# Performance work log

Hardware: AMD Instinct MI355X
Metric: run time of the kernel (lower is better)

The kernel has to match this reference:

```python
import jax, jax.numpy as jnp
import numpy as np

N, E = 20000, 320000          # nodes, edges
R, B = 9, 9                   # num_relations, num_bases
IN, HID, OUT = 128, 256, 64   # feature dims
EPS = 1e-5                    # LayerNorm eps


def layer_norm(h, gamma, beta):
    mu = jnp.mean(h, axis=-1, keepdims=True)
    var = jnp.var(h, axis=-1, keepdims=True)
    return (h - mu) * jax.lax.rsqrt(var + EPS) * gamma + beta


def rgcn_conv(x, src, dst, etype, bases, comp, root, bias, aggr):
    # basis decomposition: W_r = sum_b comp[r,b] * bases[b]
    W = jnp.einsum('rb,bio->rio', comp, bases)          # [R, in, out]
    xW = jnp.einsum('ni,rio->rno', x, W)                # [R, N, out]
    msg = xW[etype, src]                                # [E, out] gather per edge
    if aggr == 'max':
        agg = jax.ops.segment_max(msg, dst, num_segments=N)
        agg = jnp.where(jnp.isfinite(agg), agg, 0.0)    # empty segments -> 0
    else:
        agg = jax.ops.segment_sum(msg, dst, num_segments=N)
    return agg + x @ root + bias


def setup_inputs() -> dict:
    key = jax.random.key(0)
    ks = jax.random.split(key, 12)
    rn = lambda k, s, sc=0.05: jax.random.normal(k, s, jnp.float32) * sc
    return {
        'x': jax.random.normal(ks[0], (N, IN), jnp.float32),
        'edge_index': jax.random.randint(ks[1], (2, E), 0, N),
        'edge_type': jax.random.randint(ks[2], (E,), 0, R),
        # conv1 params
        'bases1': rn(ks[3], (B, IN, HID)),
        'comp1': rn(ks[4], (R, B), 0.3),
        'root1': rn(ks[5], (IN, HID)),
        'bias1': jnp.zeros((HID,), jnp.float32),
        'g1': jnp.ones((HID,), jnp.float32),
        'b1': jnp.zeros((HID,), jnp.float32),
        # conv2 params
        'bases2': rn(ks[6], (B, HID, OUT)),
        'comp2': rn(ks[7], (R, B), 0.3),
        'root2': rn(ks[8], (HID, OUT)),
        'bias2': jnp.zeros((OUT,), jnp.float32),
        'g2': jnp.ones((OUT,), jnp.float32),
        'b2': jnp.zeros((OUT,), jnp.float32),
    }


def reference(x, edge_index, edge_type, bases1, comp1, root1, bias1, g1, b1,
              bases2, comp2, root2, bias2, g2, b2):
    src, dst = edge_index[0], edge_index[1]
    h = rgcn_conv(x, src, dst, edge_type, bases1, comp1, root1, bias1, 'max')
    h = jax.nn.relu(layer_norm(h, g1, b1))
    # eval mode: edge dropout and feature dropout are identity
    h = rgcn_conv(h, src, dst, edge_type, bases2, comp2, root2, bias2, 'add')
    h = layer_norm(h, g2, b2)
    return jax.nn.log_softmax(h, axis=1)
```

## Files before the change

### kernel.cpp

```cpp
#include <hip/hip_runtime.h>
#include <math.h>

#define NN 20000
#define NE 320000
#define NREL 9
#define NBASES 9
#define D_IN 128
#define D_HID 256
#define D_OUT 64
#define LN_EPS 1e-5f

#define N1 (NREL * D_HID + D_HID)
#define N2 (NREL * D_OUT + D_OUT)
#define NBLK ((NN + 255) / 256)

typedef __attribute__((ext_vector_type(8))) short bf16x8;
typedef __attribute__((ext_vector_type(4))) float f32x4;

__device__ inline ushort f2b(float f) {
    unsigned u = __float_as_uint(f);
    return (ushort)((u + 0x7FFFu + ((u >> 16) & 1u)) >> 16);
}
__device__ inline float b2f(ushort h) { return __uint_as_float(((unsigned)h) << 16); }

__global__ __launch_bounds__(256) void prep_all(
    const float* __restrict__ bases1, const float* __restrict__ comp1, const float* __restrict__ root1,
    const float* __restrict__ bases2, const float* __restrict__ comp2, const float* __restrict__ root2,
    const float* __restrict__ x,
    ushort* __restrict__ w1t, ushort* __restrict__ w2t, ushort* __restrict__ xbf)
{
    const int SZ1 = N1 * D_IN;
    const int SZ2 = N2 * D_HID;
    const int SZX = NN * D_IN;
    int tid = blockIdx.x * 256 + threadIdx.x;
    if (tid < SZ1) {
        int n = tid >> 7, k = tid & 127;
        float s;
        if (n < NREL * D_HID) {
            int r = n >> 8, o = n & 255;
            s = 0.f;
            #pragma unroll
            for (int b = 0; b < NBASES; b++)
                s += comp1[r * NBASES + b] * bases1[(b * D_IN + k) * D_HID + o];
        } else {
            s = root1[k * D_HID + (n - NREL * D_HID)];
        }
        w1t[tid] = f2b(s);
    } else if (tid < SZ1 + SZ2) {
        int j = tid - SZ1;
        int n = j >> 8, k = j & 255;
        float s;
        if (n < NREL * D_OUT) {
            int r = n >> 6, o = n & 63;
            s = 0.f;
            #pragma unroll
            for (int b = 0; b < NBASES; b++)
                s += comp2[r * NBASES + b] * bases2[(b * D_HID + k) * D_OUT + o];
        } else {
            s = root2[k * D_OUT + (n - NREL * D_OUT)];
        }
        w2t[j] = f2b(s);
    } else if (tid < SZ1 + SZ2 + SZX) {
        int j = tid - SZ1 - SZ2;
        xbf[j] = f2b(x[j]);
    }
}

__global__ __launch_bounds__(256) void hist_dst(const int* __restrict__ dst, int* __restrict__ deg)
{
    int e = blockIdx.x * 256 + threadIdx.x;
    if (e < NE) atomicAdd(&deg[dst[e]], 1);
}

__global__ __launch_bounds__(256) void scan_blk(
    const int* __restrict__ deg, int* __restrict__ local, int* __restrict__ bsum)
{
    __shared__ int wsum[4];
    int tid = threadIdx.x, lane = tid & 63, w = tid >> 6;
    int i = blockIdx.x * 256 + tid;
    int v = (i < NN) ? deg[i] : 0;
    int x = v;
    #pragma unroll
    for (int d = 1; d < 64; d <<= 1) {
        int y = __shfl_up(x, d, 64);
        if (lane >= d) x += y;
    }
    if (lane == 63) wsum[w] = x;
    __syncthreads();
    int woff = 0;
    for (int j = 0; j < w; j++) woff += wsum[j];
    if (i < NN) local[i] = woff + x - v;
    if (tid == 255) bsum[blockIdx.x] = woff + x;
}

__global__ __launch_bounds__(64) void scan_top(const int* __restrict__ bsum, int* __restrict__ boff)
{
    int lane = threadIdx.x;
    int carry = 0;
    for (int base = 0; base < NBLK; base += 64) {
        int i = base + lane;
        int v = (i < NBLK) ? bsum[i] : 0;
        int x = v;
        #pragma unroll
        for (int d = 1; d < 64; d <<= 1) {
            int y = __shfl_up(x, d, 64);
            if (lane >= d) x += y;
        }
        if (i < NBLK) boff[i] = carry + x - v;
        carry += __shfl(x, 63, 64);
    }
}

__global__ __launch_bounds__(256) void scan_fin(
    const int* __restrict__ local, const int* __restrict__ boff,
    int* __restrict__ offs, int* __restrict__ cursor)
{
    int i = blockIdx.x * 256 + threadIdx.x;
    if (i < NN) {
        int o = local[i] + boff[i >> 8];
        offs[i] = o;
        cursor[i] = o;
    }
    if (i == NN) offs[NN] = NE;
}

__global__ __launch_bounds__(256) void scatter_ep(
    const int* __restrict__ src, const int* __restrict__ dst, const int* __restrict__ etype,
    int* __restrict__ cursor, int* __restrict__ ep1, int* __restrict__ ep2)
{
    int e = blockIdx.x * 256 + threadIdx.x;
    if (e >= NE) return;
    int d = dst[e];
    int s = src[e], r = etype[e];
    int pos = atomicAdd(&cursor[d], 1);
    ep1[pos] = s * N1 + r * D_HID;
    ep2[pos] = s * N2 + r * D_OUT;
}

__global__ __launch_bounds__(256) void gemm_bf16(
    const ushort* __restrict__ A, const ushort* __restrict__ Bt, ushort* __restrict__ C,
    int M, int N, int K)
{
    __shared__ ushort As[128 * 32];
    __shared__ ushort Bs[128 * 32];

    int tid = threadIdx.x;
    int lane = tid & 63, w = tid >> 6;
    int row0 = blockIdx.y * 128, col0 = blockIdx.x * 128;

    f32x4 acc[4][4];
    #pragma unroll
    for (int mt = 0; mt < 4; mt++)
        #pragma unroll
        for (int nt = 0; nt < 4; nt++)
            acc[mt][nt] = (f32x4){0.f, 0.f, 0.f, 0.f};

    for (int k0 = 0; k0 < K; k0 += 32) {
        #pragma unroll
        for (int cc = 0; cc < 2; cc++) {
            int c = tid + cc * 256;
            int m = c >> 2, kq = c & 3;
            int off = ((m >> 4) * 64 + (m & 15) + kq * 16) * 8;
            bf16x8 va = {0, 0, 0, 0, 0, 0, 0, 0};
            int gm = row0 + m;
            if (gm < M) va = *(const bf16x8*)&A[(size_t)gm * K + k0 + kq * 8];
            *(bf16x8*)&As[off] = va;
            bf16x8 vb = *(const bf16x8*)&Bt[(size_t)(col0 + m) * K + k0 + kq * 8];
            *(bf16x8*)&Bs[off] = vb;
        }
        __syncthreads();

        int tA = (w >> 1) * 4, tB = (w & 1) * 4;
        bf16x8 af[4], bfr[4];
        #pragma unroll
        for (int i = 0; i < 4; i++) af[i]  = *(const bf16x8*)&As[((tA + i) * 64 + lane) * 8];
        #pragma unroll
        for (int i = 0; i < 4; i++) bfr[i] = *(const bf16x8*)&Bs[((tB + i) * 64 + lane) * 8];

        #pragma unroll
        for (int mt = 0; mt < 4; mt++)
            #pragma unroll
            for (int nt = 0; nt < 4; nt++)
                acc[mt][nt] = __builtin_amdgcn_mfma_f32_16x16x32_bf16(af[mt], bfr[nt], acc[mt][nt], 0, 0, 0);
        __syncthreads();
    }

    int q = lane >> 4, cn = lane & 15;
    #pragma unroll
    for (int mt = 0; mt < 4; mt++) {
        #pragma unroll
        for (int i = 0; i < 4; i++) {
            int gr = row0 + (w >> 1) * 64 + mt * 16 + q * 4 + i;
            if (gr < M) {
                #pragma unroll
                for (int nt = 0; nt < 4; nt++) {
                    int gc = col0 + (w & 1) * 64 + nt * 16 + cn;
                    C[(size_t)gr * N + gc] = f2b(acc[mt][nt][i]);
                }
            }
        }
    }
}

__global__ __launch_bounds__(256) void gather1(
    const ushort* __restrict__ xw1, const int* __restrict__ offs, const int* __restrict__ ep1,
    const float* __restrict__ bias, const float* __restrict__ g, const float* __restrict__ b,
    ushort* __restrict__ h)
{
    int n = blockIdx.x * 4 + (threadIdx.x >> 6);
    if (n >= NN) return;
    int lane = threadIdx.x & 63;
    int lane4 = lane * 4;
    int e0 = __builtin_amdgcn_readfirstlane(offs[n]);
    int e1 = __builtin_amdgcn_readfirstlane(offs[n + 1]);

    float m0 = -INFINITY, m1 = -INFINITY, m2 = -INFINITY, m3 = -INFINITY;
    int e = e0;
    for (; e + 4 <= e1; e += 4) {
        int p0 = ep1[e + 0], p1 = ep1[e + 1], p2 = ep1[e + 2], p3 = ep1[e + 3];
        ushort4 v0 = *(const ushort4*)&xw1[(size_t)(p0 + lane4)];
        ushort4 v1 = *(const ushort4*)&xw1[(size_t)(p1 + lane4)];
        ushort4 v2 = *(const ushort4*)&xw1[(size_t)(p2 + lane4)];
        ushort4 v3 = *(const ushort4*)&xw1[(size_t)(p3 + lane4)];
        m0 = fmaxf(fmaxf(m0, fmaxf(b2f(v0.x), b2f(v1.x))), fmaxf(b2f(v2.x), b2f(v3.x)));
        m1 = fmaxf(fmaxf(m1, fmaxf(b2f(v0.y), b2f(v1.y))), fmaxf(b2f(v2.y), b2f(v3.y)));
        m2 = fmaxf(fmaxf(m2, fmaxf(b2f(v0.z), b2f(v1.z))), fmaxf(b2f(v2.z), b2f(v3.z)));
        m3 = fmaxf(fmaxf(m3, fmaxf(b2f(v0.w), b2f(v1.w))), fmaxf(b2f(v2.w), b2f(v3.w)));
    }
    for (; e < e1; e++) {
        int p = ep1[e];
        ushort4 v = *(const ushort4*)&xw1[(size_t)(p + lane4)];
        m0 = fmaxf(m0, b2f(v.x)); m1 = fmaxf(m1, b2f(v.y));
        m2 = fmaxf(m2, b2f(v.z)); m3 = fmaxf(m3, b2f(v.w));
    }
    if (e1 == e0) { m0 = m1 = m2 = m3 = 0.f; }

    ushort4 rt = *(const ushort4*)&xw1[(size_t)n * N1 + NREL * D_HID + lane4];
    int c = lane4;
    float t0 = m0 + b2f(rt.x) + bias[c + 0];
    float t1 = m1 + b2f(rt.y) + bias[c + 1];
    float t2 = m2 + b2f(rt.z) + bias[c + 2];
    float t3 = m3 + b2f(rt.w) + bias[c + 3];

    float s = t0 + t1 + t2 + t3;
    float s2 = t0 * t0 + t1 * t1 + t2 * t2 + t3 * t3;
    #pragma unroll
    for (int m = 32; m >= 1; m >>= 1) {
        s  += __shfl_xor(s,  m, 64);
        s2 += __shfl_xor(s2, m, 64);
    }
    float mu = s * (1.f / D_HID);
    float var = s2 * (1.f / D_HID) - mu * mu;
    float rs = rsqrtf(var + LN_EPS);

    ushort4 o;
    o.x = f2b(fmaxf((t0 - mu) * rs * g[c + 0] + b[c + 0], 0.f));
    o.y = f2b(fmaxf((t1 - mu) * rs * g[c + 1] + b[c + 1], 0.f));
    o.z = f2b(fmaxf((t2 - mu) * rs * g[c + 2] + b[c + 2], 0.f));
    o.w = f2b(fmaxf((t3 - mu) * rs * g[c + 3] + b[c + 3], 0.f));
    *(ushort4*)&h[(size_t)n * D_HID + c] = o;
}

__global__ __launch_bounds__(256) void gather2(
    const ushort* __restrict__ xw2, const int* __restrict__ offs, const int* __restrict__ ep2,
    const float* __restrict__ bias, const float* __restrict__ g, const float* __restrict__ b,
    float* __restrict__ out)
{
    int n = blockIdx.x * 4 + (threadIdx.x >> 6);
    if (n >= NN) return;
    int lane = threadIdx.x & 63;
    int e0 = __builtin_amdgcn_readfirstlane(offs[n]);
    int e1 = __builtin_amdgcn_readfirstlane(offs[n + 1]);

    float s = 0.f;
    int e = e0;
    for (; e + 4 <= e1; e += 4) {
        int p0 = ep2[e + 0], p1 = ep2[e + 1], p2 = ep2[e + 2], p3 = ep2[e + 3];
        float a0 = b2f(xw2[(size_t)(p0 + lane)]);
        float a1 = b2f(xw2[(size_t)(p1 + lane)]);
        float a2 = b2f(xw2[(size_t)(p2 + lane)]);
        float a3 = b2f(xw2[(size_t)(p3 + lane)]);
        s += (a0 + a1) + (a2 + a3);
    }
    for (; e < e1; e++) {
        s += b2f(xw2[(size_t)(ep2[e] + lane)]);
    }
    float v = s + b2f(xw2[(size_t)n * N2 + NREL * D_OUT + lane]) + bias[lane];

    float sm = v, s2 = v * v;
    #pragma unroll
    for (int m = 32; m >= 1; m >>= 1) {
        sm += __shfl_xor(sm, m, 64);
        s2 += __shfl_xor(s2, m, 64);
    }
    float mu = sm * (1.f / D_OUT);
    float var = s2 * (1.f / D_OUT) - mu * mu;
    float y = (v - mu) * rsqrtf(var + LN_EPS) * g[lane] + b[lane];

    float mx = y;
    #pragma unroll
    for (int m = 32; m >= 1; m >>= 1) mx = fmaxf(mx, __shfl_xor(mx, m, 64));
    float ex = __expf(y - mx);
    float se = ex;
    #pragma unroll
    for (int m = 32; m >= 1; m >>= 1) se += __shfl_xor(se, m, 64);
    out[(size_t)n * D_OUT + lane] = y - mx - logf(se);
}

extern "C" void kernel_launch(void* const* d_in, const int* in_sizes, int n_in,
                              void* d_out, int out_size, void* d_ws, size_t ws_size,
                              hipStream_t stream)
{
    const float* x      = (const float*)d_in[0];
    const int*   eidx   = (const int*)  d_in[1];
    const int*   etype  = (const int*)  d_in[2];
    const float* bases1 = (const float*)d_in[3];
    const float* comp1  = (const float*)d_in[4];
    const float* root1  = (const float*)d_in[5];
    const float* bias1  = (const float*)d_in[6];
    const float* g1     = (const float*)d_in[7];
    const float* b1     = (const float*)d_in[8];
    const float* bases2 = (const float*)d_in[9];
    const float* comp2  = (const float*)d_in[10];
    const float* root2  = (const float*)d_in[11];
    const float* bias2  = (const float*)d_in[12];
    const float* g2     = (const float*)d_in[13];
    const float* b2     = (const float*)d_in[14];

    const int* src = eidx;
    const int* dst = eidx + NE;

    char* p = (char*)d_ws;
    auto alloc = [&](size_t bytes) -> char* {
        char* r = p;
        p += (bytes + 255) & ~(size_t)255;
        return r;
    };
    ushort* xbf    = (ushort*)alloc((size_t)NN * D_IN * 2);
    ushort* w1t    = (ushort*)alloc((size_t)N1 * D_IN * 2);
    ushort* w2t    = (ushort*)alloc((size_t)N2 * D_HID * 2);
    ushort* xw1    = (ushort*)alloc((size_t)NN * N1 * 2);
    ushort* xw2    = (ushort*)alloc((size_t)NN * N2 * 2);
    ushort* h      = (ushort*)alloc((size_t)NN * D_HID * 2);
    int*    deg    = (int*)   alloc((size_t)NN * 4);
    int*    local  = (int*)   alloc((size_t)NN * 4);
    int*    bsum   = (int*)   alloc((size_t)NBLK * 4);
    int*    boff   = (int*)   alloc((size_t)NBLK * 4);
    int*    offs   = (int*)   alloc((size_t)(NN + 1) * 4);
    int*    cursor = (int*)   alloc((size_t)NN * 4);
    int*    ep1    = (int*)   alloc((size_t)NE * 4);
    int*    ep2    = (int*)   alloc((size_t)NE * 4);

    const int SZP = N1 * D_IN + N2 * D_HID + NN * D_IN;
    prep_all<<<(SZP + 255) / 256, 256, 0, stream>>>(
        bases1, comp1, root1, bases2, comp2, root2, x, w1t, w2t, xbf);

    hipMemsetAsync(deg, 0, (size_t)NN * 4, stream);
    hist_dst<<<(NE + 255) / 256, 256, 0, stream>>>(dst, deg);
    scan_blk<<<NBLK, 256, 0, stream>>>(deg, local, bsum);
    scan_top<<<1, 64, 0, stream>>>(bsum, boff);
    scan_fin<<<NBLK, 256, 0, stream>>>(local, boff, offs, cursor);
    scatter_ep<<<(NE + 255) / 256, 256, 0, stream>>>(src, dst, etype, cursor, ep1, ep2);

    gemm_bf16<<<dim3(N1 / 128, (NN + 127) / 128), 256, 0, stream>>>(xbf, w1t, xw1, NN, N1, D_IN);
    gather1<<<(NN + 3) / 4, 256, 0, stream>>>(xw1, offs, ep1, bias1, g1, b1, h);

    gemm_bf16<<<dim3(N2 / 128, (NN + 127) / 128), 256, 0, stream>>>(h, w2t, xw2, NN, N2, D_HID);
    gather2<<<(NN + 3) / 4, 256, 0, stream>>>(xw2, offs, ep2, bias2, g2, b2, (float*)d_out);
}
```

Before: 251.6 us.

## Use direct global-to-LDS loads, K=64 tiles and vectorized transposed GEMM epilogue

The bf16 GEMM now stages A and B tiles with global_load_lds (direct global-to-LDS DMA) instead of loading through registers, and doubles the K step per iteration to 64 so there are half as many barriers. The MFMA operands are swapped so each lane holds four consecutive output columns, which allows packed 8-byte stores in place of scalar 2-byte stores. Out-of-range rows are clamped to M-1 rather than zero-filled, which is safe because those rows are never stored. The LDS layout still has no swizzle, so bank conflicts on the fragment reads may remain.

```diff
diff --git a/kernel.cpp b/kernel.cpp
--- a/kernel.cpp
+++ b/kernel.cpp
@@ -22,6 +22,9 @@
     return (ushort)((u + 0x7FFFu + ((u >> 16) & 1u)) >> 16);
 }
 __device__ inline float b2f(ushort h) { return __uint_as_float(((unsigned)h) << 16); }
+__device__ inline unsigned pack2bf(float f0, float f1) {
+    return (unsigned)f2b(f0) | ((unsigned)f2b(f1) << 16);
+}
 
 __global__ __launch_bounds__(256) void prep_all(
     const float* __restrict__ bases1, const float* __restrict__ comp1, const float* __restrict__ root1,
@@ -141,11 +144,12 @@
     const ushort* __restrict__ A, const ushort* __restrict__ Bt, ushort* __restrict__ C,
     int M, int N, int K)
 {
-    __shared__ ushort As[128 * 32];
-    __shared__ ushort Bs[128 * 32];
+    __shared__ ushort As[1024 * 8];
+    __shared__ ushort Bs[1024 * 8];
 
     int tid = threadIdx.x;
     int lane = tid & 63, w = tid >> 6;
+    int wm = w >> 1, wn = w & 1;
     int row0 = blockIdx.y * 128, col0 = blockIdx.x * 128;
 
     f32x4 acc[4][4];
@@ -155,48 +159,68 @@
         for (int nt = 0; nt < 4; nt++)
             acc[mt][nt] = (f32x4){0.f, 0.f, 0.f, 0.f};
 
-    for (int k0 = 0; k0 < K; k0 += 32) {
-        #pragma unroll
-        for (int cc = 0; cc < 2; cc++) {
-            int c = tid + cc * 256;
-            int m = c >> 2, kq = c & 3;
-            int off = ((m >> 4) * 64 + (m & 15) + kq * 16) * 8;
-            bf16x8 va = {0, 0, 0, 0, 0, 0, 0, 0};
-            int gm = row0 + m;
-            if (gm < M) va = *(const bf16x8*)&A[(size_t)gm * K + k0 + kq * 8];
-            *(bf16x8*)&As[off] = va;
-            bf16x8 vb = *(const bf16x8*)&Bt[(size_t)(col0 + m) * K + k0 + kq * 8];
-            *(bf16x8*)&Bs[off] = vb;
+    for (int k0 = 0; k0 < K; k0 += 64) {
+        #pragma unroll
+        for (int it = 0; it < 4; it++) {
+            int sbase = (it * 4 + w) * 64;
+            int s = sbase + lane;
+            int g = s >> 7, rem = s & 127;
+            int kc = rem >> 4, mr = rem & 15;
+            int row = row0 + g * 16 + mr;
+            row = min(row, M - 1);
+            const ushort* ga = &A[(size_t)row * K + k0 + kc * 8];
+            __builtin_amdgcn_global_load_lds(
+                (const __attribute__((address_space(1))) unsigned int*)ga,
+                (__attribute__((address_space(3))) unsigned int*)&As[(size_t)sbase * 8],
+                16, 0, 0);
+        }
+        #pragma unroll
+        for (int it = 0; it < 4; it++) {
+            int sbase = (it * 4 + w) * 64;
+            int s = sbase + lane;
+            int g = s >> 7, rem = s & 127;
+            int kc = rem >> 4, mr = rem & 15;
+            int col = col0 + g * 16 + mr;
+            const ushort* gb = &Bt[(size_t)col * K + k0 + kc * 8];
+            __builtin_amdgcn_global_load_lds(
+                (const __attribute__((address_space(1))) unsigned int*)gb,
+                (__attribute__((address_space(3))) unsigned int*)&Bs[(size_t)sbase * 8],
+                16, 0, 0);
         }
         __syncthreads();
 
-        int tA = (w >> 1) * 4, tB = (w & 1) * 4;
-        bf16x8 af[4], bfr[4];
-        #pragma unroll
-        for (int i = 0; i < 4; i++) af[i]  = *(const bf16x8*)&As[((tA + i) * 64 + lane) * 8];
-        #pragma unroll
-        for (int i = 0; i < 4; i++) bfr[i] = *(const bf16x8*)&Bs[((tB + i) * 64 + lane) * 8];
-
-        #pragma unroll
-        for (int mt = 0; mt < 4; mt++)
+        #pragma unroll
+        for (int ks = 0; ks < 2; ks++) {
+            int fo = (ks * 4 + (lane >> 4)) * 16 + (lane & 15);
+            bf16x8 af[4], bfr[4];
+            #pragma unroll
+            for (int mt = 0; mt < 4; mt++)
+                af[mt] = *(const bf16x8*)&As[(size_t)(((wm * 4 + mt) * 128) + fo) * 8];
             #pragma unroll
             for (int nt = 0; nt < 4; nt++)
-                acc[mt][nt] = __builtin_amdgcn_mfma_f32_16x16x32_bf16(af[mt], bfr[nt], acc[mt][nt], 0, 0, 0);
+                bfr[nt] = *(const bf16x8*)&Bs[(size_t)(((wn * 4 + nt) * 128) + fo) * 8];
+            #pragma unroll
+            for (int mt = 0; mt < 4; mt++)
+                #pragma unroll
+                for (int nt = 0; nt < 4; nt++)
+                    acc[mt][nt] = __builtin_amdgcn_mfma_f32_16x16x32_bf16(
+                        bfr[nt], af[mt], acc[mt][nt], 0, 0, 0);
+        }
         __syncthreads();
     }
 
-    int q = lane >> 4, cn = lane & 15;
+    int q = lane >> 4, cm = lane & 15;
     #pragma unroll
     for (int mt = 0; mt < 4; mt++) {
-        #pragma unroll
-        for (int i = 0; i < 4; i++) {
-            int gr = row0 + (w >> 1) * 64 + mt * 16 + q * 4 + i;
-            if (gr < M) {
-                #pragma unroll
-                for (int nt = 0; nt < 4; nt++) {
-                    int gc = col0 + (w & 1) * 64 + nt * 16 + cn;
-                    C[(size_t)gr * N + gc] = f2b(acc[mt][nt][i]);
-                }
+        int gr = row0 + wm * 64 + mt * 16 + cm;
+        if (gr < M) {
+            #pragma unroll
+            for (int nt = 0; nt < 4; nt++) {
+                int gc = col0 + wn * 64 + nt * 16 + q * 4;
+                uint2 o;
+                o.x = pack2bf(acc[mt][nt][0], acc[mt][nt][1]);
+                o.y = pack2bf(acc[mt][nt][2], acc[mt][nt][3]);
+                *(uint2*)&C[(size_t)gr * N + gc] = o;
             }
         }
     }
```

Measured after the change: 267.7 us. +6.4%, slower.
